# Performance work log

Hardware: AMD Instinct MI355X
Metric: run time of the kernel (lower is better)

The kernel has to match this reference:

```python
import jax, jax.numpy as jnp
import numpy as np

B, C, H, W = 8, 256, 64, 64
NH, FF, L, K = 8, 1024, 3, 64
THR = 0.5
DH = C // NH
SCALE = 1.0 / float(np.sqrt(DH))
N = H * W


def setup_inputs() -> dict:
    key = jax.random.key(0)
    ks = jax.random.split(key, 16)
    s = 0.02
    rn = lambda k, shape: (jax.random.normal(k, shape, jnp.float32) * s)
    return {
        "x": jax.random.normal(ks[0], (B, C, H, W), jnp.float32),
        "y": jax.random.normal(ks[1], (B, C, H, W), jnp.float32),
        "proj_w": rn(ks[2], (C, 2 * C)), "proj_b": rn(ks[3], (C,)),
        "sal_w": rn(ks[4], (1, C)), "sal_b": rn(ks[5], (1,)),
        "soft_w": rn(ks[6], (2, K, C)), "soft_b": rn(ks[7], (2, K)),
        "attn_in_w": rn(ks[8], (2, L, 3 * C, C)), "attn_in_b": rn(ks[9], (2, L, 3 * C)),
        "attn_out_w": rn(ks[10], (2, L, C, C)), "attn_out_b": rn(ks[11], (2, L, C)),
        "n1_g": jnp.ones((2, L, C), jnp.float32), "n1_b": jnp.zeros((2, L, C), jnp.float32),
        "ffn_w1": rn(ks[12], (2, L, FF, C)), "ffn_b1": rn(ks[13], (2, L, FF)),
        "ffn_w2": rn(ks[14], (2, L, C, FF)), "ffn_b2": rn(ks[15], (2, L, C)),
        "n2_g": jnp.ones((2, L, C), jnp.float32), "n2_b": jnp.zeros((2, L, C), jnp.float32),
    }


def _ln(t, g, b, eps=1e-5):
    m = t.mean(-1, keepdims=True)
    v = ((t - m) ** 2).mean(-1, keepdims=True)
    return (t - m) / jnp.sqrt(v + eps) * g + b


def _layers(q, kv, p, side):
    # q: [B,N,C] pixel queries, kv: [B,K,C] soft-pooled tokens
    for l in range(L):
        iw, ib = p["attn_in_w"][side, l], p["attn_in_b"][side, l]
        qq = (q @ iw[:C].T + ib[:C]).reshape(B, -1, NH, DH)
        kk = (kv @ iw[C:2 * C].T + ib[C:2 * C]).reshape(B, K, NH, DH)
        vv = (kv @ iw[2 * C:].T + ib[2 * C:]).reshape(B, K, NH, DH)
        att = jax.nn.softmax(jnp.einsum('bnhd,bkhd->bhnk', qq, kk) * SCALE, axis=-1)
        o = jnp.einsum('bhnk,bkhd->bnhd', att, vv).reshape(B, -1, C)
        o = o @ p["attn_out_w"][side, l].T + p["attn_out_b"][side, l]
        q = _ln(q + o, p["n1_g"][side, l], p["n1_b"][side, l])
        h = jax.nn.relu(q @ p["ffn_w1"][side, l].T + p["ffn_b1"][side, l])
        h = h @ p["ffn_w2"][side, l].T + p["ffn_b2"][side, l]
        q = _ln(q + h, p["n2_g"][side, l], p["n2_b"][side, l])
    return q


def _forward(x, y, proj_w, proj_b, sal_w, sal_b, soft_w, soft_b,
             attn_in_w, attn_in_b, attn_out_w, attn_out_b, n1_g, n1_b,
             ffn_w1, ffn_b1, ffn_w2, ffn_b2, n2_g, n2_b):
    p = dict(attn_in_w=attn_in_w, attn_in_b=attn_in_b, attn_out_w=attn_out_w,
             attn_out_b=attn_out_b, n1_g=n1_g, n1_b=n1_b, ffn_w1=ffn_w1,
             ffn_b1=ffn_b1, ffn_w2=ffn_w2, ffn_b2=ffn_b2, n2_g=n2_g, n2_b=n2_b)
    xc = jnp.concatenate([x, y], axis=1)                                  # [B,2C,H,W]
    feat = jnp.einsum('oc,bchw->bohw', proj_w, xc) + proj_b[None, :, None, None]
    sal = jnp.einsum('oc,bchw->bohw', sal_w, feat) + sal_b[None, :, None, None]  # [B,1,H,W]
    heat = jax.nn.sigmoid(sal)
    fg_mask = (heat >= THR).reshape(B, 1, N)
    bg_mask = (heat < 1.0 - THR).reshape(B, 1, N)
    fmap = feat.reshape(B, C, N)
    q0 = fmap.transpose(0, 2, 1)                                          # [B,N,C]
    out = fmap
    for side, hm in ((0, heat), (1, 1.0 - heat)):
        wf = feat * hm                                                    # [B,C,H,W]
        sw = (jnp.einsum('kc,bchw->bkhw', soft_w[side], wf)
              + soft_b[side][None, :, None, None]).reshape(B, K, N)       # [B,K,N]
        pool = jnp.einsum('bkn,bcn->bkc', sw, wf.reshape(B, C, N))        # [B,K,C]
        qs = _layers(q0, pool, p, side)                                   # [B,N,C]
        mask = fg_mask if side == 0 else bg_mask
        out = jnp.where(mask, qs.transpose(0, 2, 1), out)
    # per-image skip: if no fg or no bg pixels, keep original feature
    valid = fg_mask.any(axis=(1, 2)) & bg_mask.any(axis=(1, 2))           # [B]
    out = jnp.where(valid[:, None, None], out, fmap)
    return out.reshape(B, C, H, W)


def reference(x, y, proj_w, proj_b, sal_w, sal_b, soft_w, soft_b,
              attn_in_w, attn_in_b, attn_out_w, attn_out_b, n1_g, n1_b,
              ffn_w1, ffn_b1, ffn_w2, ffn_b2, n2_g, n2_b):
    return _forward(x, y, proj_w, proj_b, sal_w, sal_b, soft_w, soft_b,
                    attn_in_w, attn_in_b, attn_out_w, attn_out_b, n1_g, n1_b,
                    ffn_w1, ffn_b1, ffn_w2, ffn_b2, n2_g, n2_b)
```

## Files before the change

kernel.cpp:

```cpp
#include <hip/hip_runtime.h>
#include <stdint.h>

#define B_ 8
#define C_ 256
#define N_ 4096
#define K_ 64
#define NH_ 8
#define FF_ 1024
#define L_ 3
#define M_ (B_*N_)
#define SCALE_ 0.17677669529663687f

typedef float f32x4 __attribute__((ext_vector_type(4)));
typedef __bf16 v8bf __attribute__((ext_vector_type(8)));

__device__ __forceinline__ float b2f(unsigned short h){
  union { uint32_t u; float f; } v; v.u = ((uint32_t)h) << 16; return v.f;
}
__device__ __forceinline__ unsigned short f2b(float f){
  union { float f; uint32_t u; } v; v.f = f;
  uint32_t r = v.u + 0x7fffu + ((v.u >> 16) & 1u);
  return (unsigned short)(r >> 16);
}
__device__ __forceinline__ void gload_lds16(const void* g, void* l){
  __builtin_amdgcn_global_load_lds(
      (const __attribute__((address_space(1))) unsigned int*)g,
      (__attribute__((address_space(3))) unsigned int*)l, 16, 0, 0);
}

__global__ __launch_bounds__(256) void k_f32_to_bf16(const float* __restrict__ src,
                                                     unsigned short* __restrict__ dst, int n){
  int i4 = (blockIdx.x*256 + threadIdx.x)*4;
  if (i4 >= n) return;
  float4 v = *(const float4*)(src + i4);
  uint32_t p0 = (uint32_t)f2b(v.x) | ((uint32_t)f2b(v.y) << 16);
  uint32_t p1 = (uint32_t)f2b(v.z) | ((uint32_t)f2b(v.w) << 16);
  *(uint2*)(dst + i4) = make_uint2(p0, p1);
}

__global__ __launch_bounds__(256) void k_build_xcT(const float* __restrict__ x,
                                                   const float* __restrict__ y,
                                                   unsigned short* __restrict__ xcT){
  __shared__ float t[32][33];
  int b = blockIdx.z;
  int n0 = blockIdx.x*32, c0 = blockIdx.y*32;
  int tx = threadIdx.x, ty = threadIdx.y;
  const float* src = (c0 < 256) ? (x + ((size_t)b*256 + c0)*N_)
                                : (y + ((size_t)b*256 + (c0-256))*N_);
  #pragma unroll
  for (int i = 0; i < 4; i++){
    int cl = ty*4 + i;
    t[cl][tx] = src[(size_t)cl*N_ + n0 + tx];
  }
  __syncthreads();
  #pragma unroll
  for (int i = 0; i < 4; i++){
    int nl = ty*4 + i;
    xcT[((size_t)b*N_ + n0 + nl)*512 + c0 + tx] = f2b(t[tx][nl]);
  }
}

__global__ __launch_bounds__(256) void k_featmir(const float* __restrict__ featT,
                                                 unsigned short* __restrict__ featbf,
                                                 unsigned short* __restrict__ featC){
  __shared__ float t[32][33];
  int b = blockIdx.z;
  int n0 = blockIdx.x*32, c0 = blockIdx.y*32;
  int tx = threadIdx.x, ty = threadIdx.y;
  #pragma unroll
  for (int i = 0; i < 4; i++){
    int nl = ty*4 + i;
    size_t m = (size_t)b*N_ + n0 + nl;
    float v = featT[m*256 + c0 + tx];
    t[nl][tx] = v;
    featbf[m*256 + c0 + tx] = f2b(v);
  }
  __syncthreads();
  #pragma unroll
  for (int i = 0; i < 4; i++){
    int cl = ty*4 + i;
    featC[((size_t)b*256 + c0 + cl)*(size_t)N_ + n0 + tx] = f2b(t[tx][cl]);
  }
}

__global__ __launch_bounds__(512) void k_compute_u(const float* __restrict__ sal_w,
                                                   const float* __restrict__ proj_w,
                                                   const float* __restrict__ proj_b,
                                                   const float* __restrict__ sal_b,
                                                   double* __restrict__ u){
  int c2 = threadIdx.x;
  double acc = 0.0;
  for (int c = 0; c < 256; ++c)
    acc += (double)sal_w[c] * (double)proj_w[(size_t)c*512 + c2];
  u[c2] = acc;
  if (c2 == 0){
    double s0 = (double)sal_b[0];
    for (int c = 0; c < 256; ++c) s0 += (double)sal_w[c] * (double)proj_b[c];
    u[512] = s0;
  }
}

__global__ __launch_bounds__(256) void k_sal_part(const float* __restrict__ x,
                                                  const float* __restrict__ y,
                                                  const double* __restrict__ u,
                                                  double* __restrict__ part){
  int pix = blockIdx.x*256 + threadIdx.x;
  int cc = blockIdx.y;
  int b = pix >> 12, n = pix & 4095;
  int c0 = cc*32;
  const float* src = (c0 < 256) ? (x + ((size_t)b*256 + c0)*N_ + n)
                                : (y + ((size_t)b*256 + (c0-256))*N_ + n);
  const double* uu = u + c0;
  double acc = 0.0;
  #pragma unroll 8
  for (int c = 0; c < 32; ++c) acc += uu[c] * (double)src[(size_t)c*N_];
  part[(size_t)cc*32768 + pix] = acc;
}

__global__ __launch_bounds__(256) void k_sal_red(const double* __restrict__ part,
                                                 const double* __restrict__ u,
                                                 float* __restrict__ heat,
                                                 int* __restrict__ counts){
  int pix = blockIdx.x*256 + threadIdx.x;
  int b = pix >> 12;
  double acc = u[512];
  #pragma unroll
  for (int cc = 0; cc < 16; cc++) acc += part[(size_t)cc*32768 + pix];
  float hf = (float)(1.0 / (1.0 + exp(-acc)));
  heat[pix] = hf;
  unsigned long long mfg = __ballot(hf >= 0.5f);
  unsigned long long mbg = __ballot(hf < 0.5f);
  if ((threadIdx.x & 63) == 0){
    atomicAdd(&counts[b*2+0], (int)__popcll(mfg));
    atomicAdd(&counts[b*2+1], (int)__popcll(mbg));
  }
}

template<int EPI>
__global__ __launch_bounds__(256) void k_gemm_bt(
    const unsigned short* __restrict__ A, const unsigned short* __restrict__ W,
    const float* __restrict__ bias, void* __restrict__ out,
    int M, int N, int K){
  __shared__ unsigned short smem[2][2][128*64];
  int tid = threadIdx.x;
  int w = tid >> 6, l = tid & 63;
  int m0 = blockIdx.x * 128, n0 = blockIdx.y * 128;
  int wr = w >> 1, wc = w & 1;
  int lr = l & 15, lk = l >> 4;
  f32x4 acc[4][4] = {};
  int nt = K >> 6;
  #pragma unroll
  for (int i = 0; i < 4; i++){
    int idx = i*256 + tid;
    int row = idx >> 3, su = ((idx & 7) ^ (row & 7))*8;
    gload_lds16(A + (size_t)(m0+row)*K + su, &smem[0][0][idx*8]);
    gload_lds16(W + (size_t)(n0+row)*K + su, &smem[0][1][idx*8]);
  }
  __syncthreads();
  for (int t = 0; t < nt; ++t){
    int cur = t & 1;
    if (t + 1 < nt){
      int k0 = (t + 1) << 6;
      #pragma unroll
      for (int i = 0; i < 4; i++){
        int idx = i*256 + tid;
        int row = idx >> 3, su = ((idx & 7) ^ (row & 7))*8;
        gload_lds16(A + (size_t)(m0+row)*K + k0 + su, &smem[cur^1][0][idx*8]);
        gload_lds16(W + (size_t)(n0+row)*K + k0 + su, &smem[cur^1][1][idx*8]);
      }
    }
    const unsigned short* ldsA = smem[cur][0];
    const unsigned short* ldsB = smem[cur][1];
    #pragma unroll
    for (int kk = 0; kk < 2; kk++){
      v8bf af[4], bfr[4];
      #pragma unroll
      for (int f = 0; f < 4; f++){
        int ra = wr*64 + f*16 + lr;
        int rb2 = wc*64 + f*16 + lr;
        int u = kk*4 + lk;
        af[f]  = *(const v8bf*)(&ldsA[ra*64 + ((u ^ (ra&7))<<3)]);
        bfr[f] = *(const v8bf*)(&ldsB[rb2*64 + ((u ^ (rb2&7))<<3)]);
      }
      #pragma unroll
      for (int fi = 0; fi < 4; fi++)
        #pragma unroll
        for (int fj = 0; fj < 4; fj++)
          acc[fi][fj] = __builtin_amdgcn_mfma_f32_16x16x32_bf16(af[fi], bfr[fj], acc[fi][fj], 0, 0, 0);
    }
    __syncthreads();
  }
  if (EPI == 1 || EPI == 2){
    unsigned short* st = &smem[0][0][0];
    #pragma unroll
    for (int fj = 0; fj < 4; fj++){
      int col = wc*64 + fj*16 + lr;
      float bv = bias[n0 + col];
      #pragma unroll
      for (int fi = 0; fi < 4; fi++){
        int rl = wr*64 + fi*16 + lk*4;
        #pragma unroll
        for (int r = 0; r < 4; r++){
          float v = acc[fi][fj][r] + bv;
          if (EPI == 1) v = fmaxf(v, 0.f);
          st[(rl + r)*136 + col] = f2b(v);
        }
      }
    }
    __syncthreads();
    #pragma unroll
    for (int it = 0; it < 8; it++){
      int idx = it*256 + tid;
      int row = idx >> 4, c8 = (idx & 15)*8;
      *(uint4*)((unsigned short*)out + (size_t)(m0+row)*N + n0 + c8)
          = *(const uint4*)&st[row*136 + c8];
    }
  } else {
    #pragma unroll
    for (int fj = 0; fj < 4; fj++){
      int col = n0 + wc*64 + fj*16 + lr;
      float bv = bias[col];
      #pragma unroll
      for (int fi = 0; fi < 4; fi++){
        int rb = m0 + wr*64 + fi*16 + lk*4;
        #pragma unroll
        for (int r = 0; r < 4; r++){
          float v = acc[fi][fj][r] + bv;
          if (EPI == 3){
            int row = rb + r;
            ((unsigned short*)out)[((size_t)(row>>6)*256 + col)*64 + (row&63)] = f2b(v);
          } else {
            ((float*)out)[(size_t)(rb + r)*N + col] = v;
          }
        }
      }
    }
  }
}

__global__ __launch_bounds__(256) void k_ffn(
    const unsigned short* __restrict__ qb, const unsigned short* __restrict__ W1g,
    const float* __restrict__ b1g, const unsigned short* __restrict__ W2g,
    const float* __restrict__ b2g, unsigned short* __restrict__ outb){
  __shared__ unsigned short smem[73728];
  unsigned short* sA  = smem;
  unsigned short* sW1 = smem + 32768;
  unsigned short* sW2 = smem + 49152;
  unsigned short* sH  = smem + 65536;
  int tid = threadIdx.x, w = tid >> 6, l = tid & 63;
  int m0 = blockIdx.x * 128;
  int wrM = w >> 1, wcF = w & 1;
  int lr = l & 15, lk = l >> 4;
  #pragma unroll
  for (int i = 0; i < 16; i++){
    int idx = i*256 + tid;
    int row = idx >> 5, g = idx & 31;
    int su = (g & 24) | ((g & 7) ^ (row & 7));
    gload_lds16(qb + (size_t)(m0+row)*256 + su*8, &sA[idx*8]);
  }
  f32x4 acc[4][8] = {};
  for (int cc = 0; cc < 16; ++cc){
    int f0 = cc*64;
    #pragma unroll
    for (int i = 0; i < 8; i++){
      int idx = i*256 + tid;
      int row = idx >> 5, g = idx & 31;
      int su = (g & 24) | ((g & 7) ^ (row & 7));
      gload_lds16(W1g + (size_t)(f0+row)*256 + su*8, &sW1[idx*8]);
    }
    #pragma unroll
    for (int i = 0; i < 8; i++){
      int idx = i*256 + tid;
      int row = idx >> 3, g = idx & 7;
      int su = g ^ (row & 7);
      gload_lds16(W2g + (size_t)row*1024 + f0 + su*8, &sW2[idx*8]);
    }
    __syncthreads();
    f32x4 hacc[4][2] = {};
    #pragma unroll
    for (int ks = 0; ks < 8; ks++){
      v8bf af[4], bf[2];
      int g = ks*4 + lk;
      #pragma unroll
      for (int f = 0; f < 4; f++){
        int ra = wrM*64 + f*16 + lr;
        af[f] = *(const v8bf*)&sA[ra*256 + (((g & 24) | ((g & 7) ^ (ra & 7)))<<3)];
      }
      #pragma unroll
      for (int f = 0; f < 2; f++){
        int rf = wcF*32 + f*16 + lr;
        bf[f] = *(const v8bf*)&sW1[rf*256 + (((g & 24) | ((g & 7) ^ (rf & 7)))<<3)];
      }
      #pragma unroll
      for (int fi = 0; fi < 4; fi++)
        #pragma unroll
        for (int fj = 0; fj < 2; fj++)
          hacc[fi][fj] = __builtin_amdgcn_mfma_f32_16x16x32_bf16(af[fi], bf[fj], hacc[fi][fj], 0, 0, 0);
    }
    #pragma unroll
    for (int fj = 0; fj < 2; fj++){
      int fc = wcF*32 + fj*16 + lr;
      float b1v = b1g[f0 + fc];
      #pragma unroll
      for (int fi = 0; fi < 4; fi++){
        int mr0 = wrM*64 + fi*16 + lk*4;
        #pragma unroll
        for (int r = 0; r < 4; r++){
          float v = fmaxf(hacc[fi][fj][r] + b1v, 0.f);
          int mr = mr0 + r;
          sH[mr*64 + (((fc >> 3) ^ (mr & 7))<<3) + (fc & 7)] = f2b(v);
        }
      }
    }
    __syncthreads();
    #pragma unroll
    for (int ks2 = 0; ks2 < 2; ks2++){
      v8bf ha[4], wb[8];
      int g = ks2*4 + lk;
      #pragma unroll
      for (int f = 0; f < 4; f++){
        int rh = wrM*64 + f*16 + lr;
        ha[f] = *(const v8bf*)&sH[rh*64 + ((g ^ (rh & 7))<<3)];
      }
      #pragma unroll
      for (int f = 0; f < 8; f++){
        int rc = wcF*128 + f*16 + lr;
        wb[f] = *(const v8bf*)&sW2[rc*64 + ((g ^ (rc & 7))<<3)];
      }
      #pragma unroll
      for (int fi = 0; fi < 4; fi++)
        #pragma unroll
        for (int fc = 0; fc < 8; fc++)
          acc[fi][fc] = __builtin_amdgcn_mfma_f32_16x16x32_bf16(ha[fi], wb[fc], acc[fi][fc], 0, 0, 0);
    }
    __syncthreads();
  }
  unsigned short* st = smem;
  #pragma unroll
  for (int fc = 0; fc < 8; fc++){
    int col = wcF*128 + fc*16 + lr;
    float bv = b2g[col];
    #pragma unroll
    for (int fi = 0; fi < 4; fi++){
      int rl = wrM*64 + fi*16 + lk*4;
      #pragma unroll
      for (int r = 0; r < 4; r++)
        st[(rl + r)*264 + col] = f2b(acc[fi][fc][r] + bv);
    }
  }
  __syncthreads();
  #pragma unroll
  for (int it = 0; it < 16; it++){
    int idx = it*256 + tid;
    int row = idx >> 5, c8 = (idx & 31)*8;
    *(uint4*)(outb + (size_t)(m0+row)*256 + c8) = *(const uint4*)&st[row*264 + c8];
  }
}

__global__ __launch_bounds__(256) void k_swh(const float* __restrict__ g_all,
                                             const float* __restrict__ heat,
                                             const float* __restrict__ soft_b,
                                             unsigned short* __restrict__ swh){
  __shared__ float gl[64*129];
  __shared__ float hml[64];
  int tid = threadIdx.x;
  int blk = blockIdx.x;
  size_t m0 = (size_t)blk*64;
  int b = (int)(m0 >> 12), n0 = (int)(m0 & 4095);
  #pragma unroll
  for (int i = 0; i < 32; i++){
    int idx = i*256 + tid;
    int row = idx >> 7, col = idx & 127;
    gl[row*129 + col] = g_all[(m0 + row)*128 + col];
  }
  if (tid < 64) hml[tid] = heat[(size_t)b*4096 + n0 + tid];
  __syncthreads();
  int k = tid >> 2, j0 = (tid & 3)*16;
  #pragma unroll
  for (int s = 0; s < 2; s++){
    float sb = soft_b[s*64 + k];
    unsigned short vals[16];
    #pragma unroll
    for (int j = 0; j < 16; j++){
      int n = j0 + j;
      float h = hml[n];
      float hm = s ? (1.0f - h) : h;
      vals[j] = f2b((gl[n*129 + s*64 + k]*hm + sb)*hm);
    }
    unsigned short* dst = swh + (((size_t)b*2 + s)*64 + k)*4096 + n0 + j0;
    uint4 o0, o1;
    o0.x = vals[0] | ((uint32_t)vals[1]<<16);  o0.y = vals[2] | ((uint32_t)vals[3]<<16);
    o0.z = vals[4] | ((uint32_t)vals[5]<<16);  o0.w = vals[6] | ((uint32_t)vals[7]<<16);
    o1.x = vals[8] | ((uint32_t)vals[9]<<16);  o1.y = vals[10]| ((uint32_t)vals[11]<<16);
    o1.z = vals[12]| ((uint32_t)vals[13]<<16); o1.w = vals[14]| ((uint32_t)vals[15]<<16);
    *(uint4*)dst = o0;
    *(uint4*)(dst + 8) = o1;
  }
}

__global__ __launch_bounds__(256) void k_poolgemm(
    const unsigned short* __restrict__ swh, const unsigned short* __restrict__ featC,
    float* __restrict__ pp){
  __shared__ unsigned short ldsA[128*64];
  __shared__ unsigned short ldsB[128*64];
  int tid = threadIdx.x;
  int w = tid >> 6, l = tid & 63;
  int kc = blockIdx.x, nt = blockIdx.y, b = blockIdx.z;
  int wr = w >> 1, wc = w & 1;
  int lr = l & 15, lk = l >> 4;
  const unsigned short* A = swh  + (size_t)b*128*4096 + kc*512;
  const unsigned short* W = featC + ((size_t)b*256 + nt*128)*4096 + kc*512;
  f32x4 acc[4][4] = {};
  for (int k0 = 0; k0 < 512; k0 += 64){
    #pragma unroll
    for (int i = 0; i < 4; i++){
      int idx = i*256 + tid;
      int row = idx >> 3, su = (idx & 7) ^ (row & 7);
      gload_lds16(A + (size_t)row*4096 + k0 + su*8, &ldsA[idx*8]);
    }
    #pragma unroll
    for (int i = 0; i < 4; i++){
      int idx = i*256 + tid;
      int row = idx >> 3, su = (idx & 7) ^ (row & 7);
      gload_lds16(W + (size_t)row*4096 + k0 + su*8, &ldsB[idx*8]);
    }
    __syncthreads();
    #pragma unroll
    for (int kk = 0; kk < 2; kk++){
      v8bf af[4], bfr[4];
      #pragma unroll
      for (int f = 0; f < 4; f++){
        int ra = wr*64 + f*16 + lr;
        int rb2 = wc*64 + f*16 + lr;
        int u = kk*4 + lk;
        af[f]  = *(const v8bf*)(&ldsA[ra*64 + ((u ^ (ra&7))<<3)]);
        bfr[f] = *(const v8bf*)(&ldsB[rb2*64 + ((u ^ (rb2&7))<<3)]);
      }
      #pragma unroll
      for (int fi = 0; fi < 4; fi++)
        #pragma unroll
        for (int fj = 0; fj < 4; fj++)
          acc[fi][fj] = __builtin_amdgcn_mfma_f32_16x16x32_bf16(af[fi], bfr[fj], acc[fi][fj], 0, 0, 0);
    }
    __syncthreads();
  }
  float* dst = pp + ((size_t)kc*8 + b)*128*256;
  #pragma unroll
  for (int fj = 0; fj < 4; fj++){
    int col = nt*128 + wc*64 + fj*16 + lr;
    #pragma unroll
    for (int fi = 0; fi < 4; fi++){
      int rb = wr*64 + fi*16 + lk*4;
      #pragma unroll
      for (int r = 0; r < 4; r++)
        dst[(size_t)(rb + r)*256 + col] = acc[fi][fj][r];
    }
  }
}

__global__ __launch_bounds__(256) void k_pool2b(const float* __restrict__ pp,
                                                unsigned short* __restrict__ pool_bf_s){
  int bk = blockIdx.x, side = blockIdx.y, c = threadIdx.x;
  int b = bk >> 6, k = bk & 63;
  float s = 0.f;
  #pragma unroll
  for (int kc = 0; kc < 8; kc++)
    s += pp[(((size_t)kc*8 + b)*128 + side*64 + k)*256 + c];
  pool_bf_s[((size_t)side*512 + bk)*256 + c] = f2b(s);
}

__global__ __launch_bounds__(256) void k_attn2(
    const unsigned short* __restrict__ qq, const unsigned short* __restrict__ kk,
    const unsigned short* __restrict__ vvT, unsigned short* __restrict__ obf){
  __shared__ unsigned short sk[64*256];
  __shared__ unsigned short svT[256*64];
  __shared__ unsigned short sp[4][16*64];
  __shared__ unsigned short sow[4][16*32];
  int tid = threadIdx.x, w = tid >> 6, l = tid & 63;
  int blk = blockIdx.x, b = blk >> 6;
  int l15 = l & 15, lg = l >> 4;
  const uint4* ksrc = (const uint4*)(kk + (size_t)b*64*256);
  #pragma unroll
  for (int i = 0; i < 8; i++){
    int u = i*256 + tid;
    int row = u >> 5, j = u & 31;
    *(uint4*)&sk[row*256 + ((j ^ (row&7))<<3)] = ksrc[u];
  }
  const uint4* vsrc = (const uint4*)(vvT + (size_t)b*256*64);
  #pragma unroll
  for (int i = 0; i < 8; i++){
    int u = i*256 + tid;
    int row = u >> 3, j = u & 7;
    *(uint4*)&svT[row*64 + ((j ^ (row&7))<<3)] = vsrc[u];
  }
  __syncthreads();
  size_t qrow = (size_t)blk*64 + w*16 + l15;
  for (int h = 0; h < 8; h++){
    v8bf aq = *(const v8bf*)(qq + qrow*256 + h*32 + lg*8);
    f32x4 s[4];
    #pragma unroll
    for (int kt = 0; kt < 4; kt++){
      int row = kt*16 + l15;
      v8bf bk = *(const v8bf*)&sk[row*256 + (((h*4 + lg) ^ (row&7))<<3)];
      f32x4 z = {};
      s[kt] = __builtin_amdgcn_mfma_f32_16x16x32_bf16(aq, bk, z, 0, 0, 0);
    }
    #pragma unroll
    for (int r = 0; r < 4; r++){
      float v0 = s[0][r]*SCALE_, v1 = s[1][r]*SCALE_;
      float v2 = s[2][r]*SCALE_, v3 = s[3][r]*SCALE_;
      float mx = fmaxf(fmaxf(v0, v1), fmaxf(v2, v3));
      mx = fmaxf(mx, __shfl_xor(mx, 1));
      mx = fmaxf(mx, __shfl_xor(mx, 2));
      mx = fmaxf(mx, __shfl_xor(mx, 4));
      mx = fmaxf(mx, __shfl_xor(mx, 8));
      float e0 = __expf(v0-mx), e1 = __expf(v1-mx);
      float e2 = __expf(v2-mx), e3 = __expf(v3-mx);
      float sum = e0+e1+e2+e3;
      sum += __shfl_xor(sum, 1); sum += __shfl_xor(sum, 2);
      sum += __shfl_xor(sum, 4); sum += __shfl_xor(sum, 8);
      float inv = 1.0f/sum;
      s[0][r] = e0*inv; s[1][r] = e1*inv; s[2][r] = e2*inv; s[3][r] = e3*inv;
    }
    #pragma unroll
    for (int kt = 0; kt < 4; kt++){
      int colu = kt*2 + (l15>>3);
      #pragma unroll
      for (int r = 0; r < 4; r++){
        int row = lg*4 + r;
        sp[w][row*64 + ((colu ^ (row&7))<<3) + (l&7)] = f2b(s[kt][r]);
      }
    }
    f32x4 o[2] = {};
    #pragma unroll
    for (int k2 = 0; k2 < 2; k2++){
      v8bf pa = *(const v8bf*)&sp[w][l15*64 + (((k2*4 + lg) ^ (l15&7))<<3)];
      #pragma unroll
      for (int dt = 0; dt < 2; dt++){
        int vrow = h*32 + dt*16 + l15;
        v8bf bv = *(const v8bf*)&svT[vrow*64 + (((k2*4 + lg) ^ (vrow&7))<<3)];
        o[dt] = __builtin_amdgcn_mfma_f32_16x16x32_bf16(pa, bv, o[dt], 0, 0, 0);
      }
    }
    #pragma unroll
    for (int dt = 0; dt < 2; dt++)
      #pragma unroll
      for (int r = 0; r < 4; r++)
        sow[w][(lg*4 + r)*32 + dt*16 + l15] = f2b(o[dt][r]);
    uint4 ov = *(const uint4*)&sow[w][l15*32 + lg*8];
    *(uint4*)(obf + qrow*256 + h*32 + lg*8) = ov;
  }
}

template<int RF32>
__global__ __launch_bounds__(256) void k_ln2(
    const void* __restrict__ resid, const unsigned short* __restrict__ delta,
    const float* __restrict__ g, const float* __restrict__ bta,
    unsigned short* __restrict__ qout){
  int wv = threadIdx.x >> 6, l = threadIdx.x & 63;
  size_t m = (size_t)blockIdx.x*4 + wv;
  uint2 dv = *(const uint2*)(delta + m*256 + l*4);
  float d0 = b2f((unsigned short)(dv.x & 0xffff)), d1 = b2f((unsigned short)(dv.x >> 16));
  float d2 = b2f((unsigned short)(dv.y & 0xffff)), d3 = b2f((unsigned short)(dv.y >> 16));
  float x0, x1, x2, x3;
  if (RF32){
    float4 rv = *(const float4*)((const float*)resid + m*256 + l*4);
    x0 = rv.x+d0; x1 = rv.y+d1; x2 = rv.z+d2; x3 = rv.w+d3;
  } else {
    uint2 rv = *(const uint2*)((const unsigned short*)resid + m*256 + l*4);
    x0 = b2f((unsigned short)(rv.x & 0xffff)) + d0;
    x1 = b2f((unsigned short)(rv.x >> 16)) + d1;
    x2 = b2f((unsigned short)(rv.y & 0xffff)) + d2;
    x3 = b2f((unsigned short)(rv.y >> 16)) + d3;
  }
  float s = x0+x1+x2+x3;
  float ss = x0*x0+x1*x1+x2*x2+x3*x3;
  #pragma unroll
  for (int off = 32; off; off >>= 1){
    s  += __shfl_xor(s, off);
    ss += __shfl_xor(ss, off);
  }
  float mean = s * (1.0f/256.0f);
  float var = ss * (1.0f/256.0f) - mean*mean;
  float rstd = 1.0f / sqrtf(var + 1e-5f);
  float4 gv = *(const float4*)(g + l*4);
  float4 bv = *(const float4*)(bta + l*4);
  float y0 = (x0-mean)*rstd*gv.x + bv.x;
  float y1 = (x1-mean)*rstd*gv.y + bv.y;
  float y2 = (x2-mean)*rstd*gv.z + bv.z;
  float y3 = (x3-mean)*rstd*gv.w + bv.w;
  uint32_t p0 = (uint32_t)f2b(y0) | ((uint32_t)f2b(y1)<<16);
  uint32_t p1 = (uint32_t)f2b(y2) | ((uint32_t)f2b(y3)<<16);
  *(uint2*)(qout + m*256 + l*4) = make_uint2(p0,p1);
}

__global__ __launch_bounds__(256) void k_select(
    const unsigned short* __restrict__ qA, const unsigned short* __restrict__ qB,
    const float* __restrict__ featT, const float* __restrict__ heat,
    const int* __restrict__ counts, float* __restrict__ out){
  __shared__ float t[32][33];
  int b = blockIdx.z;
  int n0 = blockIdx.x*32, c0 = blockIdx.y*32;
  int tx = threadIdx.x, ty = threadIdx.y;
  bool valid = (counts[b*2] > 0) && (counts[b*2+1] > 0);
  #pragma unroll
  for (int i = 0; i < 4; i++){
    int nl = ty*4+i;
    size_t m = (size_t)b*4096 + n0 + nl;
    float v;
    if (!valid) v = featT[m*256 + c0 + tx];
    else {
      bool fg = heat[(size_t)b*4096 + n0 + nl] >= 0.5f;
      v = fg ? b2f(qA[m*256 + c0 + tx]) : b2f(qB[m*256 + c0 + tx]);
    }
    t[nl][tx] = v;
  }
  __syncthreads();
  #pragma unroll
  for (int i = 0; i < 4; i++){
    int cl = ty*4+i;
    out[((size_t)b*256 + c0 + cl)*4096 + n0 + tx] = t[tx][cl];
  }
}

extern "C" void kernel_launch(void* const* d_in, const int* in_sizes, int n_in,
                              void* d_out, int out_size, void* d_ws, size_t ws_size,
                              hipStream_t stream){
  const float* x         = (const float*)d_in[0];
  const float* y         = (const float*)d_in[1];
  const float* proj_w    = (const float*)d_in[2];
  const float* proj_b    = (const float*)d_in[3];
  const float* sal_w     = (const float*)d_in[4];
  const float* sal_b     = (const float*)d_in[5];
  const float* soft_w    = (const float*)d_in[6];
  const float* soft_b    = (const float*)d_in[7];
  const float* attn_in_w = (const float*)d_in[8];
  const float* attn_in_b = (const float*)d_in[9];
  const float* attn_out_w= (const float*)d_in[10];
  const float* attn_out_b= (const float*)d_in[11];
  const float* n1_g      = (const float*)d_in[12];
  const float* n1_b      = (const float*)d_in[13];
  const float* ffn_w1    = (const float*)d_in[14];
  const float* ffn_b1    = (const float*)d_in[15];
  const float* ffn_w2    = (const float*)d_in[16];
  const float* ffn_b2    = (const float*)d_in[17];
  const float* n2_g      = (const float*)d_in[18];
  const float* n2_b      = (const float*)d_in[19];
  float* out = (float*)d_out;

  char* p = (char*)d_ws;
  auto alloc = [&](size_t bytes){ char* r = p; p += (bytes + 255) & ~(size_t)255; return r; };
  unsigned short* hbf   = (unsigned short*)alloc((size_t)M_*FF_*2);
  unsigned short* xcT   = hbf;
  unsigned short* qq_bf = hbf;
  float* featT = (float*)alloc((size_t)M_*C_*4);
  unsigned short* qAb = (unsigned short*)alloc((size_t)M_*C_*2);
  unsigned short* swh = qAb;
  unsigned short* qBb = (unsigned short*)alloc((size_t)M_*C_*2);
  unsigned short* obf = (unsigned short*)alloc((size_t)M_*C_*2);
  unsigned short* featC = obf;
  unsigned short* featbf = (unsigned short*)alloc((size_t)M_*C_*2);
  unsigned short* tmpb = (unsigned short*)alloc((size_t)M_*C_*2);
  float* g_all = (float*)tmpb;
  float* pp    = (float*)alloc((size_t)8*8*128*256*4);
  double* salp = (double*)pp;
  unsigned short* pool_bf_s = (unsigned short*)alloc((size_t)2*512*256*2);
  unsigned short* kk_bf = (unsigned short*)alloc((size_t)B_*K_*C_*2);
  unsigned short* vvT_bf= (unsigned short*)alloc((size_t)B_*C_*K_*2);
  float* heat = (float*)alloc((size_t)B_*N_*4);
  double* u   = (double*)alloc(513*8);
  int* counts = (int*)alloc(64);
  float* zbias = (float*)alloc(512);
  unsigned short* projw_bf = (unsigned short*)alloc((size_t)C_*512*2);
  unsigned short* aiw_bf = (unsigned short*)alloc((size_t)2*L_*768*C_*2);
  unsigned short* aow_bf = (unsigned short*)alloc((size_t)2*L_*C_*C_*2);
  unsigned short* f1w_bf = (unsigned short*)alloc((size_t)2*L_*FF_*C_*2);
  unsigned short* f2w_bf = (unsigned short*)alloc((size_t)2*L_*C_*FF_*2);
  unsigned short* sw2_bf = (unsigned short*)alloc((size_t)2*K_*C_*2);

  hipMemsetAsync(counts, 0, 64, stream);
  hipMemsetAsync(zbias, 0, 512, stream);
  k_compute_u<<<1, 512, 0, stream>>>(sal_w, proj_w, proj_b, sal_b, u);
  k_sal_part<<<dim3(128, 16), 256, 0, stream>>>(x, y, u, salp);
  k_sal_red<<<128, 256, 0, stream>>>(salp, u, heat, counts);

  auto conv = [&](const float* s, unsigned short* d, size_t n){
    k_f32_to_bf16<<<(unsigned)((n/4 + 255)/256), 256, 0, stream>>>(s, d, (int)n);
  };
  conv(proj_w,     projw_bf, (size_t)C_*512);
  conv(attn_in_w,  aiw_bf,   (size_t)2*L_*768*C_);
  conv(attn_out_w, aow_bf,   (size_t)2*L_*C_*C_);
  conv(ffn_w1,     f1w_bf,   (size_t)2*L_*FF_*C_);
  conv(ffn_w2,     f2w_bf,   (size_t)2*L_*C_*FF_);
  conv(soft_w,     sw2_bf,   (size_t)2*K_*C_);

  k_build_xcT<<<dim3(N_/32, 512/32, B_), dim3(32,8), 0, stream>>>(x, y, xcT);
  k_gemm_bt<0><<<dim3(M_/128, C_/128), 256, 0, stream>>>(xcT, projw_bf, proj_b, featT, M_, C_, 512);
  k_featmir<<<dim3(N_/32, C_/32, B_), dim3(32,8), 0, stream>>>(featT, featbf, featC);

  k_gemm_bt<0><<<dim3(M_/128, 1), 256, 0, stream>>>(featbf, sw2_bf, zbias, g_all, M_, 128, C_);
  k_swh<<<M_/64, 256, 0, stream>>>(g_all, heat, soft_b, swh);
  k_poolgemm<<<dim3(8, 2, B_), 256, 0, stream>>>(swh, featC, pp);
  k_pool2b<<<dim3(512, 2), 256, 0, stream>>>(pp, pool_bf_s);

  for (int side = 0; side < 2; ++side){
    unsigned short* qb = side ? qBb : qAb;
    const unsigned short* poolS = pool_bf_s + (size_t)side*512*256;
    for (int lyr = 0; lyr < L_; ++lyr){
      int sl = side*L_ + lyr;
      const unsigned short* iw = aiw_bf + (size_t)sl*768*C_;
      const float* ib = attn_in_b + (size_t)sl*768;
      const unsigned short* qin = (lyr == 0) ? featbf : qb;
      k_gemm_bt<2><<<dim3(M_/128, C_/128), 256, 0, stream>>>(qin, iw, ib, qq_bf, M_, C_, C_);
      k_gemm_bt<2><<<dim3((B_*K_)/128, C_/128), 256, 0, stream>>>(poolS, iw + 256*C_, ib + 256, kk_bf, B_*K_, C_, C_);
      k_gemm_bt<3><<<dim3((B_*K_)/128, C_/128), 256, 0, stream>>>(poolS, iw + 512*C_, ib + 512, vvT_bf, B_*K_, C_, C_);
      k_attn2<<<M_/64, 256, 0, stream>>>(qq_bf, kk_bf, vvT_bf, obf);
      k_gemm_bt<2><<<dim3(M_/128, C_/128), 256, 0, stream>>>(obf, aow_bf + (size_t)sl*C_*C_, attn_out_b + (size_t)sl*C_, tmpb, M_, C_, C_);
      if (lyr == 0)
        k_ln2<1><<<M_/4, 256, 0, stream>>>(featT, tmpb, n1_g + (size_t)sl*C_, n1_b + (size_t)sl*C_, qb);
      else
        k_ln2<0><<<M_/4, 256, 0, stream>>>(qb, tmpb, n1_g + (size_t)sl*C_, n1_b + (size_t)sl*C_, qb);
      k_ffn<<<M_/128, 256, 0, stream>>>(qb, f1w_bf + (size_t)sl*FF_*C_, ffn_b1 + (size_t)sl*FF_,
                                        f2w_bf + (size_t)sl*C_*FF_, ffn_b2 + (size_t)sl*C_, tmpb);
      k_ln2<0><<<M_/4, 256, 0, stream>>>(qb, tmpb, n2_g + (size_t)sl*C_, n2_b + (size_t)sl*C_, qb);
    }
  }
  k_select<<<dim3(N_/32, C_/32, B_), dim3(32,8), 0, stream>>>(qAb, qBb, featT, heat, counts, out);
}
```

Measured before the change: 970.6 us.

## Double waves in fused FFN kernel and prefetch next weight chunk early

The fused FFN kernel now runs 512 threads (8 waves) per block instead of 256. Each wave owns a 64-row by 16-wide slice of the hidden chunk and a 64-row by 64-column slice of the output, which halves the per-wave accumulator count. The next W1 chunk is loaded right after the first GEMM's barrier, and the next W2 chunk after the second GEMM's barrier, so these loads overlap with compute instead of sitting at the top of each iteration. This aims to improve latency hiding and MFMA issue, at the cost of more barrier participants and extra LDS reads of the shared A and H tiles per wave.

```diff
diff --git a/kernel.cpp b/kernel.cpp
--- a/kernel.cpp
+++ b/kernel.cpp
@@ -238,7 +238,7 @@
   }
 }
 
-__global__ __launch_bounds__(256) void k_ffn(
+__global__ __launch_bounds__(512) void k_ffn(
     const unsigned short* __restrict__ qb, const unsigned short* __restrict__ W1g,
     const float* __restrict__ b1g, const unsigned short* __restrict__ W2g,
     const float* __restrict__ b2g, unsigned short* __restrict__ outb){
@@ -247,102 +247,116 @@
   unsigned short* sW1 = smem + 32768;
   unsigned short* sW2 = smem + 49152;
   unsigned short* sH  = smem + 65536;
-  int tid = threadIdx.x, w = tid >> 6, l = tid & 63;
+  int tid = threadIdx.x;
+  int w = tid >> 6, l = tid & 63;
   int m0 = blockIdx.x * 128;
-  int wrM = w >> 1, wcF = w & 1;
+  int wm = w >> 2;
+  int wf = w & 3;
   int lr = l & 15, lk = l >> 4;
-  #pragma unroll
-  for (int i = 0; i < 16; i++){
-    int idx = i*256 + tid;
+
+  #pragma unroll
+  for (int i = 0; i < 8; i++){
+    int idx = i*512 + tid;
     int row = idx >> 5, g = idx & 31;
     int su = (g & 24) | ((g & 7) ^ (row & 7));
     gload_lds16(qb + (size_t)(m0+row)*256 + su*8, &sA[idx*8]);
   }
-  f32x4 acc[4][8] = {};
+  #pragma unroll
+  for (int i = 0; i < 4; i++){
+    int idx = i*512 + tid;
+    int row = idx >> 5, g = idx & 31;
+    int su = (g & 24) | ((g & 7) ^ (row & 7));
+    gload_lds16(W1g + (size_t)row*256 + su*8, &sW1[idx*8]);
+  }
+  #pragma unroll
+  for (int i = 0; i < 4; i++){
+    int idx = i*512 + tid;
+    int row = idx >> 3, g = idx & 7;
+    int su = g ^ (row & 7);
+    gload_lds16(W2g + (size_t)row*1024 + su*8, &sW2[idx*8]);
+  }
+  __syncthreads();
+
+  f32x4 acc[4][4] = {};
   for (int cc = 0; cc < 16; ++cc){
-    int f0 = cc*64;
-    #pragma unroll
-    for (int i = 0; i < 8; i++){
-      int idx = i*256 + tid;
-      int row = idx >> 5, g = idx & 31;
-      int su = (g & 24) | ((g & 7) ^ (row & 7));
-      gload_lds16(W1g + (size_t)(f0+row)*256 + su*8, &sW1[idx*8]);
-    }
-    #pragma unroll
-    for (int i = 0; i < 8; i++){
-      int idx = i*256 + tid;
-      int row = idx >> 3, g = idx & 7;
-      int su = g ^ (row & 7);
-      gload_lds16(W2g + (size_t)row*1024 + f0 + su*8, &sW2[idx*8]);
-    }
-    __syncthreads();
-    f32x4 hacc[4][2] = {};
+    f32x4 hacc[4] = {};
     #pragma unroll
     for (int ks = 0; ks < 8; ks++){
-      v8bf af[4], bf[2];
       int g = ks*4 + lk;
+      int rf = wf*16 + lr;
+      v8bf bf1 = *(const v8bf*)&sW1[rf*256 + (((g & 24) | ((g & 7) ^ (rf & 7)))<<3)];
       #pragma unroll
       for (int f = 0; f < 4; f++){
-        int ra = wrM*64 + f*16 + lr;
-        af[f] = *(const v8bf*)&sA[ra*256 + (((g & 24) | ((g & 7) ^ (ra & 7)))<<3)];
-      }
-      #pragma unroll
-      for (int f = 0; f < 2; f++){
-        int rf = wcF*32 + f*16 + lr;
-        bf[f] = *(const v8bf*)&sW1[rf*256 + (((g & 24) | ((g & 7) ^ (rf & 7)))<<3)];
-      }
-      #pragma unroll
-      for (int fi = 0; fi < 4; fi++)
-        #pragma unroll
-        for (int fj = 0; fj < 2; fj++)
-          hacc[fi][fj] = __builtin_amdgcn_mfma_f32_16x16x32_bf16(af[fi], bf[fj], hacc[fi][fj], 0, 0, 0);
-    }
-    #pragma unroll
-    for (int fj = 0; fj < 2; fj++){
-      int fc = wcF*32 + fj*16 + lr;
-      float b1v = b1g[f0 + fc];
+        int ra = wm*64 + f*16 + lr;
+        v8bf af = *(const v8bf*)&sA[ra*256 + (((g & 24) | ((g & 7) ^ (ra & 7)))<<3)];
+        hacc[f] = __builtin_amdgcn_mfma_f32_16x16x32_bf16(af, bf1, hacc[f], 0, 0, 0);
+      }
+    }
+    {
+      int fc = wf*16 + lr;
+      float b1v = b1g[cc*64 + fc];
       #pragma unroll
       for (int fi = 0; fi < 4; fi++){
-        int mr0 = wrM*64 + fi*16 + lk*4;
+        int mr0 = wm*64 + fi*16 + lk*4;
         #pragma unroll
         for (int r = 0; r < 4; r++){
-          float v = fmaxf(hacc[fi][fj][r] + b1v, 0.f);
+          float v = fmaxf(hacc[fi][r] + b1v, 0.f);
           int mr = mr0 + r;
           sH[mr*64 + (((fc >> 3) ^ (mr & 7))<<3) + (fc & 7)] = f2b(v);
         }
       }
     }
     __syncthreads();
+    if (cc + 1 < 16){
+      int f0n = (cc+1)*64;
+      #pragma unroll
+      for (int i = 0; i < 4; i++){
+        int idx = i*512 + tid;
+        int row = idx >> 5, g = idx & 31;
+        int su = (g & 24) | ((g & 7) ^ (row & 7));
+        gload_lds16(W1g + (size_t)(f0n+row)*256 + su*8, &sW1[idx*8]);
+      }
+    }
     #pragma unroll
     for (int ks2 = 0; ks2 < 2; ks2++){
-      v8bf ha[4], wb[8];
       int g = ks2*4 + lk;
+      v8bf ha[4], wb[4];
       #pragma unroll
       for (int f = 0; f < 4; f++){
-        int rh = wrM*64 + f*16 + lr;
+        int rh = wm*64 + f*16 + lr;
         ha[f] = *(const v8bf*)&sH[rh*64 + ((g ^ (rh & 7))<<3)];
       }
       #pragma unroll
-      for (int f = 0; f < 8; f++){
-        int rc = wcF*128 + f*16 + lr;
+      for (int f = 0; f < 4; f++){
+        int rc = wf*64 + f*16 + lr;
         wb[f] = *(const v8bf*)&sW2[rc*64 + ((g ^ (rc & 7))<<3)];
       }
       #pragma unroll
       for (int fi = 0; fi < 4; fi++)
         #pragma unroll
-        for (int fc = 0; fc < 8; fc++)
+        for (int fc = 0; fc < 4; fc++)
           acc[fi][fc] = __builtin_amdgcn_mfma_f32_16x16x32_bf16(ha[fi], wb[fc], acc[fi][fc], 0, 0, 0);
     }
     __syncthreads();
+    if (cc + 1 < 16){
+      int f0n = (cc+1)*64;
+      #pragma unroll
+      for (int i = 0; i < 4; i++){
+        int idx = i*512 + tid;
+        int row = idx >> 3, g = idx & 7;
+        int su = g ^ (row & 7);
+        gload_lds16(W2g + (size_t)row*1024 + f0n + su*8, &sW2[idx*8]);
+      }
+    }
   }
   unsigned short* st = smem;
   #pragma unroll
-  for (int fc = 0; fc < 8; fc++){
-    int col = wcF*128 + fc*16 + lr;
+  for (int fc = 0; fc < 4; fc++){
+    int col = wf*64 + fc*16 + lr;
     float bv = b2g[col];
     #pragma unroll
     for (int fi = 0; fi < 4; fi++){
-      int rl = wrM*64 + fi*16 + lk*4;
+      int rl = wm*64 + fi*16 + lk*4;
       #pragma unroll
       for (int r = 0; r < 4; r++)
         st[(rl + r)*264 + col] = f2b(acc[fi][fc][r] + bv);
@@ -350,8 +364,8 @@
   }
   __syncthreads();
   #pragma unroll
-  for (int it = 0; it < 16; it++){
-    int idx = it*256 + tid;
+  for (int it = 0; it < 8; it++){
+    int idx = it*512 + tid;
     int row = idx >> 5, c8 = (idx & 31)*8;
     *(uint4*)(outb + (size_t)(m0+row)*256 + c8) = *(const uint4*)&st[row*264 + c8];
   }
@@ -720,7 +734,7 @@
         k_ln2<1><<<M_/4, 256, 0, stream>>>(featT, tmpb, n1_g + (size_t)sl*C_, n1_b + (size_t)sl*C_, qb);
       else
         k_ln2<0><<<M_/4, 256, 0, stream>>>(qb, tmpb, n1_g + (size_t)sl*C_, n1_b + (size_t)sl*C_, qb);
-      k_ffn<<<M_/128, 256, 0, stream>>>(qb, f1w_bf + (size_t)sl*FF_*C_, ffn_b1 + (size_t)sl*FF_,
+      k_ffn<<<M_/128, 512, 0, stream>>>(qb, f1w_bf + (size_t)sl*FF_*C_, ffn_b1 + (size_t)sl*FF_,
                                         f2w_bf + (size_t)sl*C_*FF_, ffn_b2 + (size_t)sl*C_, tmpb);
       k_ln2<0><<<M_/4, 256, 0, stream>>>(qb, tmpb, n2_g + (size_t)sl*C_, n2_b + (size_t)sl*C_, qb);
     }
```

After: 855.4 us. 1.13x faster.
